# Kernel optimization log

Measured on AMD Instinct MI355X. Metric: run time of the kernel, lower is better.

Reference implementation:

```python
import jax, jax.numpy as jnp
import numpy as np

NUM_EXPERTS = 8
TOP_K = 2


def setup_inputs() -> dict:
    key = jax.random.key(0)
    ks = jax.random.split(key, 6)
    B, S, H, I, E = 2, 2048, 1024, 4096, NUM_EXPERTS
    scale_g = 1.0 / np.sqrt(H)
    scale1 = 1.0 / np.sqrt(H)
    scale2 = 1.0 / np.sqrt(I)
    return {
        "x": jax.random.normal(ks[0], (B, S, H), dtype=jnp.float32),
        "Wg": jax.random.normal(ks[1], (E, H), dtype=jnp.float32) * scale_g,
        "W1": jax.random.normal(ks[2], (E, I, H), dtype=jnp.float32) * scale1,
        "b1": jax.random.normal(ks[3], (E, I), dtype=jnp.float32) * scale1,
        "W2": jax.random.normal(ks[4], (E, H, I), dtype=jnp.float32) * scale2,
        "b2": jax.random.normal(ks[5], (E, H), dtype=jnp.float32) * scale2,
    }


def reference(x, Wg, W1, b1, W2, b2):
    # x: [B, S, H]
    B, S, H = x.shape
    flat = x.reshape(-1, H)  # [T, H], T = B*S

    # --- Router: gate logits -> softmax -> top-k -> renormalize ---
    logits = flat @ Wg.T                      # [T, E]
    probs = jax.nn.softmax(logits, axis=-1)   # [T, E]
    w, sel = jax.lax.top_k(probs, TOP_K)      # [T, K], [T, K]
    w = w / jnp.sum(w, axis=-1, keepdims=True)

    # --- Dispatch / expert MLP / weighted combine ---
    # Equivalent to argsort dispatch + per-expert chunks + combine:
    # each token receives sum_k w[t,k] * expert_{sel[t,k]}(flat[t]).
    out = jnp.zeros_like(flat)
    for e in range(NUM_EXPERTS):
        h = jax.nn.gelu(flat @ W1[e].T + b1[e], approximate=False)  # [T, I]
        y = h @ W2[e].T + b2[e]                                     # [T, H]
        we = jnp.sum(jnp.where(sel == e, w, 0.0), axis=-1)          # [T]
        out = out + we[:, None] * y
    return out.reshape(B, S, H)
```

## Files before the change

### kernel.cpp

```cpp
#include <hip/hip_runtime.h>
#include <hip/hip_bf16.h>
#include <math.h>

#define T_TOK 4096
#define H_DIM 1024
#define I_DIM 4096
#define NEXP 8
#define RMAX 8192

#if __has_builtin(__builtin_amdgcn_global_load_lds)
#define USE_GLL 1
#else
#define USE_GLL 0
#endif

typedef __attribute__((ext_vector_type(4))) float f32x4;
typedef __attribute__((ext_vector_type(8))) short short8;

#if USE_GLL
typedef __attribute__((address_space(1))) const void gconst_t;
typedef __attribute__((address_space(3))) void lds_t;
#endif

static __device__ __forceinline__ short bfc(float f) {
    return __builtin_bit_cast(short, __float2bfloat16(f));
}
static __device__ __forceinline__ short8 cvt8(float4 a, float4 b) {
    short8 r;
    r[0] = bfc(a.x); r[1] = bfc(a.y); r[2] = bfc(a.z); r[3] = bfc(a.w);
    r[4] = bfc(b.x); r[5] = bfc(b.y); r[6] = bfc(b.z); r[7] = bfc(b.w);
    return r;
}

#define W1_CHUNKS (NEXP * I_DIM * H_DIM / 8)
#define X_CHUNKS  (T_TOK * H_DIM / 8)

__global__ __launch_bounds__(256) void prep_kernel(
    const float* __restrict__ W1, const float* __restrict__ W2, const float* __restrict__ x,
    unsigned short* __restrict__ w1b, unsigned short* __restrict__ w2b, unsigned short* __restrict__ xb,
    int* __restrict__ counts)
{
    int stride = gridDim.x * blockDim.x;
    for (int i = blockIdx.x * blockDim.x + threadIdx.x; i < W1_CHUNKS; i += stride) {
        const float4* s1 = (const float4*)W1 + 2 * i;
        ((short8*)w1b)[i] = cvt8(s1[0], s1[1]);
        const float4* s2 = (const float4*)W2 + 2 * i;
        ((short8*)w2b)[i] = cvt8(s2[0], s2[1]);
        if (i < X_CHUNKS) {
            const float4* sx = (const float4*)x + 2 * i;
            ((short8*)xb)[i] = cvt8(sx[0], sx[1]);
        }
        if (i < 16) counts[i] = 0;
    }
}

__global__ __launch_bounds__(256) void router_kernel(
    const float* __restrict__ x, const float* __restrict__ Wg,
    int* __restrict__ sel, float* __restrict__ wtk, int* __restrict__ counts)
{
    __shared__ float wg[NEXP * H_DIM];
    int tid = threadIdx.x;
    float4* wg4 = (float4*)wg;
    const float4* Wg4 = (const float4*)Wg;
    for (int i = tid; i < NEXP * H_DIM / 4; i += 256) wg4[i] = Wg4[i];
    __syncthreads();

    int wid = tid >> 6, lane = tid & 63;
    int tok = blockIdx.x * 4 + wid;

    float acc[NEXP];
#pragma unroll
    for (int e = 0; e < NEXP; ++e) acc[e] = 0.f;

    const float* xr = x + tok * H_DIM;
#pragma unroll
    for (int it = 0; it < H_DIM / 64; ++it) {
        int h = it * 64 + lane;
        float xv = xr[h];
#pragma unroll
        for (int e = 0; e < NEXP; ++e) acc[e] += xv * wg[e * H_DIM + h];
    }
#pragma unroll
    for (int e = 0; e < NEXP; ++e) {
#pragma unroll
        for (int off = 32; off > 0; off >>= 1)
            acc[e] += __shfl_xor(acc[e], off);
    }
    if (lane == 0) {
        int e0 = 0; float l0 = acc[0];
#pragma unroll
        for (int e = 1; e < NEXP; ++e) if (acc[e] > l0) { l0 = acc[e]; e0 = e; }
        int e1 = -1; float l1 = -1e30f;
#pragma unroll
        for (int e = 0; e < NEXP; ++e) if (e != e0 && acc[e] > l1) { l1 = acc[e]; e1 = e; }
        float w0 = 1.f / (1.f + expf(l1 - l0));
        float w1 = 1.f - w0;
        sel[tok * 2 + 0] = e0; sel[tok * 2 + 1] = e1;
        wtk[tok * 2 + 0] = w0; wtk[tok * 2 + 1] = w1;
        atomicAdd(&counts[e0], 1);
        atomicAdd(&counts[e1], 1);
    }
}

__global__ void offsets_kernel(const int* __restrict__ counts, int* __restrict__ offsets) {
    if (threadIdx.x == 0) {
        int s = 0;
        for (int e = 0; e < NEXP; ++e) { offsets[e] = s; s += counts[e]; }
        offsets[NEXP] = s;
    }
}

__global__ void scatter_kernel(const int* __restrict__ sel,
                               const int* __restrict__ offsets, int* __restrict__ cursors,
                               int* __restrict__ rowTok, int* __restrict__ rowOfTok)
{
    int idx = blockIdx.x * blockDim.x + threadIdx.x;
    if (idx >= 2 * T_TOK) return;
    int t = idx >> 1;
    int e = sel[idx];
    int pos = atomicAdd(&cursors[e], 1);
    int row = offsets[e] + pos;
    rowTok[row] = t;
    rowOfTok[idx] = row;
}


__global__ __launch_bounds__(256) void gemm1_kernel(
    const unsigned short* __restrict__ xb, const unsigned short* __restrict__ w1b,
    const float* __restrict__ b1,
    const int* __restrict__ offsets, const int* __restrict__ rowTok,
    unsigned short* __restrict__ hbuf)
{
    int e = blockIdx.z;
    int rowBeg = offsets[e], rowEnd = offsets[e + 1];
    int mbase = rowBeg + blockIdx.y * 128;
    if (mbase >= rowEnd) return;
    int ntile = blockIdx.x;

    __shared__ __align__(16) short As[128 * 64];
    __shared__ __align__(16) short Bs[128 * 64];

    int tid = threadIdx.x;
    int wid = tid >> 6, lane = tid & 63;
    int wr = wid >> 1, wc = wid & 1;
    f32x4 acc[4][4] = {};

#if USE_GLL
    const unsigned short* aSrc[4];
    const unsigned short* bSrc[4];
#pragma unroll
    for (int i = 0; i < 4; ++i) {
        int cc = i * 64 + lane;
        int r = wid * 32 + (cc >> 3);
        int s = cc & 7;
        int chunk = s ^ (r & 7);
        int crow = min(mbase + r, rowEnd - 1);
        aSrc[i] = xb + (size_t)rowTok[crow] * H_DIM + chunk * 8;
        bSrc[i] = w1b + (size_t)e * (I_DIM * H_DIM) + (size_t)(ntile * 128 + r) * H_DIM + chunk * 8;
    }
    short* aDst = As + wid * 2048;
    short* bDst = Bs + wid * 2048;
#else
    int srow = tid >> 1, shalf = tid & 1;
    int crow = min(mbase + srow, rowEnd - 1);
    const unsigned short* aBase = xb + (size_t)rowTok[crow] * H_DIM + shalf * 32;
    const unsigned short* bBase = w1b + (size_t)e * (I_DIM * H_DIM) + (size_t)(ntile * 128 + srow) * H_DIM + shalf * 32;
#endif

    for (int kt = 0; kt < H_DIM / 64; ++kt) {
#if USE_GLL
#pragma unroll
        for (int i = 0; i < 4; ++i) {
            __builtin_amdgcn_global_load_lds((gconst_t*)(aSrc[i] + kt * 64), (lds_t*)(aDst + i * 512), 16, 0, 0);
            __builtin_amdgcn_global_load_lds((gconst_t*)(bSrc[i] + kt * 64), (lds_t*)(bDst + i * 512), 16, 0, 0);
        }
        __syncthreads();
#else
        short8 avv[4], bvv[4];
#pragma unroll
        for (int c = 0; c < 4; ++c) {
            avv[c] = ((const short8*)(aBase + kt * 64))[c];
            bvv[c] = ((const short8*)(bBase + kt * 64))[c];
        }
        __syncthreads();
#pragma unroll
        for (int c = 0; c < 4; ++c) {
            int sw = ((shalf * 4 + c) ^ (srow & 7)) << 4;
            *(short8*)((char*)As + srow * 128 + sw) = avv[c];
            *(short8*)((char*)Bs + srow * 128 + sw) = bvv[c];
        }
        __syncthreads();
#endif
#pragma unroll
        for (int ks = 0; ks < 2; ++ks) {
            short8 af[4], bfr[4];
            int kchunk = ks * 4 + (lane >> 4);
#pragma unroll
            for (int m = 0; m < 4; ++m) {
                int r = wr * 64 + m * 16 + (lane & 15);
                af[m] = *(const short8*)((const char*)As + r * 128 + ((kchunk ^ (r & 7)) << 4));
            }
#pragma unroll
            for (int n = 0; n < 4; ++n) {
                int r = wc * 64 + n * 16 + (lane & 15);
                bfr[n] = *(const short8*)((const char*)Bs + r * 128 + ((kchunk ^ (r & 7)) << 4));
            }
#pragma unroll
            for (int m = 0; m < 4; ++m)
#pragma unroll
                for (int n = 0; n < 4; ++n)
                    acc[m][n] = __builtin_amdgcn_mfma_f32_16x16x32_bf16(af[m], bfr[n], acc[m][n], 0, 0, 0);
        }
        __syncthreads();
    }

    const float* b1e = b1 + e * I_DIM + ntile * 128;
#pragma unroll
    for (int n = 0; n < 4; ++n) {
        int colL = wc * 64 + n * 16 + (lane & 15);
        float bias = b1e[colL];
        int colG = ntile * 128 + colL;
#pragma unroll
        for (int m = 0; m < 4; ++m) {
            int baseR = mbase + wr * 64 + m * 16 + ((lane >> 4) << 2);
            f32x4 f = acc[m][n];
#pragma unroll
            for (int j = 0; j < 4; ++j) {
                int r = baseR + j;
                if (r < rowEnd) {
                    float v = f[j] + bias;
                    v = 0.5f * v * (1.f + erff(v * 0.70710678118654752f));
                    hbuf[(size_t)r * I_DIM + colG] = (unsigned short)bfc(v);
                }
            }
        }
    }
}

__global__ __launch_bounds__(256) void gemm2_kernel(
    const unsigned short* __restrict__ hbuf, const unsigned short* __restrict__ w2b,
    const float* __restrict__ b2,
    const int* __restrict__ offsets,
    float* __restrict__ ybuf)
{
    int e = blockIdx.z;
    int rowBeg = offsets[e], rowEnd = offsets[e + 1];
    int mbase = rowBeg + blockIdx.y * 128;
    if (mbase >= rowEnd) return;
    int ntile = blockIdx.x;

    __shared__ __align__(16) short As[128 * 64];
    __shared__ __align__(16) short Bs[128 * 64];

    int tid = threadIdx.x;
    int wid = tid >> 6, lane = tid & 63;
    int wr = wid >> 1, wc = wid & 1;
    f32x4 acc[4][4] = {};

#if USE_GLL
    const unsigned short* aSrc[4];
    const unsigned short* bSrc[4];
#pragma unroll
    for (int i = 0; i < 4; ++i) {
        int cc = i * 64 + lane;
        int r = wid * 32 + (cc >> 3);
        int s = cc & 7;
        int chunk = s ^ (r & 7);
        int crow = min(mbase + r, rowEnd - 1);
        aSrc[i] = hbuf + (size_t)crow * I_DIM + chunk * 8;
        bSrc[i] = w2b + (size_t)e * (H_DIM * I_DIM) + (size_t)(ntile * 128 + r) * I_DIM + chunk * 8;
    }
    short* aDst = As + wid * 2048;
    short* bDst = Bs + wid * 2048;
#else
    int srow = tid >> 1, shalf = tid & 1;
    int crow = min(mbase + srow, rowEnd - 1);
    const unsigned short* aBase = hbuf + (size_t)crow * I_DIM + shalf * 32;
    const unsigned short* bBase = w2b + (size_t)e * (H_DIM * I_DIM) + (size_t)(ntile * 128 + srow) * I_DIM + shalf * 32;
#endif

    for (int kt = 0; kt < I_DIM / 64; ++kt) {
#if USE_GLL
#pragma unroll
        for (int i = 0; i < 4; ++i) {
            __builtin_amdgcn_global_load_lds((gconst_t*)(aSrc[i] + kt * 64), (lds_t*)(aDst + i * 512), 16, 0, 0);
            __builtin_amdgcn_global_load_lds((gconst_t*)(bSrc[i] + kt * 64), (lds_t*)(bDst + i * 512), 16, 0, 0);
        }
        __syncthreads();
#else
        short8 avv[4], bvv[4];
#pragma unroll
        for (int c = 0; c < 4; ++c) {
            avv[c] = ((const short8*)(aBase + kt * 64))[c];
            bvv[c] = ((const short8*)(bBase + kt * 64))[c];
        }
        __syncthreads();
#pragma unroll
        for (int c = 0; c < 4; ++c) {
            int sw = ((shalf * 4 + c) ^ (srow & 7)) << 4;
            *(short8*)((char*)As + srow * 128 + sw) = avv[c];
            *(short8*)((char*)Bs + srow * 128 + sw) = bvv[c];
        }
        __syncthreads();
#endif
#pragma unroll
        for (int ks = 0; ks < 2; ++ks) {
            short8 af[4], bfr[4];
            int kchunk = ks * 4 + (lane >> 4);
#pragma unroll
            for (int m = 0; m < 4; ++m) {
                int r = wr * 64 + m * 16 + (lane & 15);
                af[m] = *(const short8*)((const char*)As + r * 128 + ((kchunk ^ (r & 7)) << 4));
            }
#pragma unroll
            for (int n = 0; n < 4; ++n) {
                int r = wc * 64 + n * 16 + (lane & 15);
                bfr[n] = *(const short8*)((const char*)Bs + r * 128 + ((kchunk ^ (r & 7)) << 4));
            }
#pragma unroll
            for (int m = 0; m < 4; ++m)
#pragma unroll
                for (int n = 0; n < 4; ++n)
                    acc[m][n] = __builtin_amdgcn_mfma_f32_16x16x32_bf16(af[m], bfr[n], acc[m][n], 0, 0, 0);
        }
        __syncthreads();
    }

    const float* b2e = b2 + e * H_DIM + ntile * 128;
#pragma unroll
    for (int m = 0; m < 4; ++m) {
        int baseR = mbase + wr * 64 + m * 16 + ((lane >> 4) << 2);
#pragma unroll
        for (int n = 0; n < 4; ++n) {
            int colL = wc * 64 + n * 16 + (lane & 15);
            float bias = b2e[colL];
            int colG = ntile * 128 + colL;
            f32x4 f = acc[m][n];
#pragma unroll
            for (int j = 0; j < 4; ++j) {
                int r = baseR + j;
                if (r < rowEnd)
                    ybuf[(size_t)r * H_DIM + colG] = f[j] + bias;
            }
        }
    }
}

__global__ __launch_bounds__(256) void combine_kernel(
    const float* __restrict__ ybuf, const int* __restrict__ rowOfTok,
    const float* __restrict__ wtk, float* __restrict__ out)
{
    int t = blockIdx.x;
    int r0 = rowOfTok[2 * t], r1 = rowOfTok[2 * t + 1];
    float w0 = wtk[2 * t], w1 = wtk[2 * t + 1];
    const float4* y0 = (const float4*)(ybuf + (size_t)r0 * H_DIM);
    const float4* y1 = (const float4*)(ybuf + (size_t)r1 * H_DIM);
    float4* o = (float4*)(out + (size_t)t * H_DIM);
    int c = threadIdx.x;
    float4 a = y0[c], b = y1[c];
    float4 r;
    r.x = w0 * a.x + w1 * b.x;
    r.y = w0 * a.y + w1 * b.y;
    r.z = w0 * a.z + w1 * b.z;
    r.w = w0 * a.w + w1 * b.w;
    o[c] = r;
}

extern "C" void kernel_launch(void* const* d_in, const int* in_sizes, int n_in,
                              void* d_out, int out_size, void* d_ws, size_t ws_size,
                              hipStream_t stream) {
    const float* x  = (const float*)d_in[0];
    const float* Wg = (const float*)d_in[1];
    const float* W1 = (const float*)d_in[2];
    const float* b1 = (const float*)d_in[3];
    const float* W2 = (const float*)d_in[4];
    const float* b2 = (const float*)d_in[5];
    float* out = (float*)d_out;

    int* sel       = (int*)d_ws;
    float* wtk     = (float*)(sel + 2 * T_TOK);
    int* counts    = (int*)(wtk + 2 * T_TOK);
    int* cursors   = counts + 8;
    int* offsets   = cursors + 8;
    int* rowTok    = offsets + 16;
    int* rowOfTok  = rowTok + RMAX;
    unsigned short* xb   = (unsigned short*)(rowOfTok + RMAX);
    unsigned short* w1b  = xb + (size_t)T_TOK * H_DIM;
    unsigned short* w2b  = w1b + (size_t)NEXP * I_DIM * H_DIM;
    unsigned short* hbuf = w2b + (size_t)NEXP * H_DIM * I_DIM;
    float* ybuf          = (float*)(hbuf + (size_t)RMAX * I_DIM);

    prep_kernel<<<2048, 256, 0, stream>>>(W1, W2, x, w1b, w2b, xb, counts);
    router_kernel<<<T_TOK / 4, 256, 0, stream>>>(x, Wg, sel, wtk, counts);
    offsets_kernel<<<1, 64, 0, stream>>>(counts, offsets);
    scatter_kernel<<<(2 * T_TOK + 255) / 256, 256, 0, stream>>>(sel, offsets, cursors, rowTok, rowOfTok);
    gemm1_kernel<<<dim3(I_DIM / 128, 64, NEXP), 256, 0, stream>>>(xb, w1b, b1, offsets, rowTok, hbuf);
    gemm2_kernel<<<dim3(H_DIM / 128, 64, NEXP), 256, 0, stream>>>(hbuf, w2b, b2, offsets, ybuf);
    combine_kernel<<<T_TOK, 256, 0, stream>>>(ybuf, rowOfTok, wtk, out);
}
```

Before: 847.9 us.

## Double-buffer LDS tiles in expert GEMMs to overlap loads with MFMA

Both expert GEMM kernels now use two LDS buffers per operand. The next K-tile is prefetched, via global_load_lds or through registers, while MFMAs run on the current tile, which hides global load latency and removes one barrier per iteration on the GLL path. LDS use per block doubles to 64KB, which can lower occupancy. The prep kernel grid is also doubled.

Measured after the change: 849.3 us. Within noise of the previous version (+0.2%).

```diff
diff --git a/kernel.cpp b/kernel.cpp
--- a/kernel.cpp
+++ b/kernel.cpp
@@ -137,8 +137,8 @@
     if (mbase >= rowEnd) return;
     int ntile = blockIdx.x;
 
-    __shared__ __align__(16) short As[128 * 64];
-    __shared__ __align__(16) short Bs[128 * 64];
+    __shared__ __align__(16) short As[2][128 * 64];
+    __shared__ __align__(16) short Bs[2][128 * 64];
 
     int tid = threadIdx.x;
     int wid = tid >> 6, lane = tid & 63;
@@ -158,39 +158,55 @@
         aSrc[i] = xb + (size_t)rowTok[crow] * H_DIM + chunk * 8;
         bSrc[i] = w1b + (size_t)e * (I_DIM * H_DIM) + (size_t)(ntile * 128 + r) * H_DIM + chunk * 8;
     }
-    short* aDst = As + wid * 2048;
-    short* bDst = Bs + wid * 2048;
+#pragma unroll
+    for (int i = 0; i < 4; ++i) {
+        __builtin_amdgcn_global_load_lds((gconst_t*)aSrc[i], (lds_t*)(As[0] + wid * 2048 + i * 512), 16, 0, 0);
+        __builtin_amdgcn_global_load_lds((gconst_t*)bSrc[i], (lds_t*)(Bs[0] + wid * 2048 + i * 512), 16, 0, 0);
+    }
+    __syncthreads();
 #else
     int srow = tid >> 1, shalf = tid & 1;
-    int crow = min(mbase + srow, rowEnd - 1);
-    const unsigned short* aBase = xb + (size_t)rowTok[crow] * H_DIM + shalf * 32;
+    int crow0 = min(mbase + srow, rowEnd - 1);
+    const unsigned short* aBase = xb + (size_t)rowTok[crow0] * H_DIM + shalf * 32;
     const unsigned short* bBase = w1b + (size_t)e * (I_DIM * H_DIM) + (size_t)(ntile * 128 + srow) * H_DIM + shalf * 32;
-#endif
-
-    for (int kt = 0; kt < H_DIM / 64; ++kt) {
+    {
+        short8 avv[4], bvv[4];
+#pragma unroll
+        for (int c = 0; c < 4; ++c) { avv[c] = ((const short8*)aBase)[c]; bvv[c] = ((const short8*)bBase)[c]; }
+#pragma unroll
+        for (int c = 0; c < 4; ++c) {
+            int sw = ((shalf * 4 + c) ^ (srow & 7)) << 4;
+            *(short8*)((char*)As[0] + srow * 128 + sw) = avv[c];
+            *(short8*)((char*)Bs[0] + srow * 128 + sw) = bvv[c];
+        }
+        __syncthreads();
+    }
+#endif
+
+    const int NT = H_DIM / 64;
+    for (int kt = 0; kt < NT; ++kt) {
+        int cur = kt & 1;
 #if USE_GLL
-#pragma unroll
-        for (int i = 0; i < 4; ++i) {
-            __builtin_amdgcn_global_load_lds((gconst_t*)(aSrc[i] + kt * 64), (lds_t*)(aDst + i * 512), 16, 0, 0);
-            __builtin_amdgcn_global_load_lds((gconst_t*)(bSrc[i] + kt * 64), (lds_t*)(bDst + i * 512), 16, 0, 0);
-        }
-        __syncthreads();
+        if (kt + 1 < NT) {
+            int nxt = cur ^ 1;
+#pragma unroll
+            for (int i = 0; i < 4; ++i) {
+                __builtin_amdgcn_global_load_lds((gconst_t*)(aSrc[i] + (kt + 1) * 64), (lds_t*)(As[nxt] + wid * 2048 + i * 512), 16, 0, 0);
+                __builtin_amdgcn_global_load_lds((gconst_t*)(bSrc[i] + (kt + 1) * 64), (lds_t*)(Bs[nxt] + wid * 2048 + i * 512), 16, 0, 0);
+            }
+        }
 #else
         short8 avv[4], bvv[4];
-#pragma unroll
-        for (int c = 0; c < 4; ++c) {
-            avv[c] = ((const short8*)(aBase + kt * 64))[c];
-            bvv[c] = ((const short8*)(bBase + kt * 64))[c];
-        }
-        __syncthreads();
-#pragma unroll
-        for (int c = 0; c < 4; ++c) {
-            int sw = ((shalf * 4 + c) ^ (srow & 7)) << 4;
-            *(short8*)((char*)As + srow * 128 + sw) = avv[c];
-            *(short8*)((char*)Bs + srow * 128 + sw) = bvv[c];
-        }
-        __syncthreads();
-#endif
+        if (kt + 1 < NT) {
+#pragma unroll
+            for (int c = 0; c < 4; ++c) {
+                avv[c] = ((const short8*)(aBase + (kt + 1) * 64))[c];
+                bvv[c] = ((const short8*)(bBase + (kt + 1) * 64))[c];
+            }
+        }
+#endif
+        const short* curA = As[cur];
+        const short* curB = Bs[cur];
 #pragma unroll
         for (int ks = 0; ks < 2; ++ks) {
             short8 af[4], bfr[4];
@@ -198,12 +214,12 @@
 #pragma unroll
             for (int m = 0; m < 4; ++m) {
                 int r = wr * 64 + m * 16 + (lane & 15);
-                af[m] = *(const short8*)((const char*)As + r * 128 + ((kchunk ^ (r & 7)) << 4));
+                af[m] = *(const short8*)((const char*)curA + r * 128 + ((kchunk ^ (r & 7)) << 4));
             }
 #pragma unroll
             for (int n = 0; n < 4; ++n) {
                 int r = wc * 64 + n * 16 + (lane & 15);
-                bfr[n] = *(const short8*)((const char*)Bs + r * 128 + ((kchunk ^ (r & 7)) << 4));
+                bfr[n] = *(const short8*)((const char*)curB + r * 128 + ((kchunk ^ (r & 7)) << 4));
             }
 #pragma unroll
             for (int m = 0; m < 4; ++m)
@@ -211,6 +227,18 @@
                 for (int n = 0; n < 4; ++n)
                     acc[m][n] = __builtin_amdgcn_mfma_f32_16x16x32_bf16(af[m], bfr[n], acc[m][n], 0, 0, 0);
         }
+#if !USE_GLL
+        if (kt + 1 < NT) {
+            __syncthreads();
+            int nxt = cur ^ 1;
+#pragma unroll
+            for (int c = 0; c < 4; ++c) {
+                int sw = ((shalf * 4 + c) ^ (srow & 7)) << 4;
+                *(short8*)((char*)As[nxt] + srow * 128 + sw) = avv[c];
+                *(short8*)((char*)Bs[nxt] + srow * 128 + sw) = bvv[c];
+            }
+        }
+#endif
         __syncthreads();
     }
 
@@ -249,8 +277,8 @@
     if (mbase >= rowEnd) return;
     int ntile = blockIdx.x;
 
-    __shared__ __align__(16) short As[128 * 64];
-    __shared__ __align__(16) short Bs[128 * 64];
+    __shared__ __align__(16) short As[2][128 * 64];
+    __shared__ __align__(16) short Bs[2][128 * 64];
 
     int tid = threadIdx.x;
     int wid = tid >> 6, lane = tid & 63;
@@ -270,39 +298,55 @@
         aSrc[i] = hbuf + (size_t)crow * I_DIM + chunk * 8;
         bSrc[i] = w2b + (size_t)e * (H_DIM * I_DIM) + (size_t)(ntile * 128 + r) * I_DIM + chunk * 8;
     }
-    short* aDst = As + wid * 2048;
-    short* bDst = Bs + wid * 2048;
+#pragma unroll
+    for (int i = 0; i < 4; ++i) {
+        __builtin_amdgcn_global_load_lds((gconst_t*)aSrc[i], (lds_t*)(As[0] + wid * 2048 + i * 512), 16, 0, 0);
+        __builtin_amdgcn_global_load_lds((gconst_t*)bSrc[i], (lds_t*)(Bs[0] + wid * 2048 + i * 512), 16, 0, 0);
+    }
+    __syncthreads();
 #else
     int srow = tid >> 1, shalf = tid & 1;
-    int crow = min(mbase + srow, rowEnd - 1);
-    const unsigned short* aBase = hbuf + (size_t)crow * I_DIM + shalf * 32;
+    int crow0 = min(mbase + srow, rowEnd - 1);
+    const unsigned short* aBase = hbuf + (size_t)crow0 * I_DIM + shalf * 32;
     const unsigned short* bBase = w2b + (size_t)e * (H_DIM * I_DIM) + (size_t)(ntile * 128 + srow) * I_DIM + shalf * 32;
-#endif
-
-    for (int kt = 0; kt < I_DIM / 64; ++kt) {
+    {
+        short8 avv[4], bvv[4];
+#pragma unroll
+        for (int c = 0; c < 4; ++c) { avv[c] = ((const short8*)aBase)[c]; bvv[c] = ((const short8*)bBase)[c]; }
+#pragma unroll
+        for (int c = 0; c < 4; ++c) {
+            int sw = ((shalf * 4 + c) ^ (srow & 7)) << 4;
+            *(short8*)((char*)As[0] + srow * 128 + sw) = avv[c];
+            *(short8*)((char*)Bs[0] + srow * 128 + sw) = bvv[c];
+        }
+        __syncthreads();
+    }
+#endif
+
+    const int NT = I_DIM / 64;
+    for (int kt = 0; kt < NT; ++kt) {
+        int cur = kt & 1;
 #if USE_GLL
-#pragma unroll
-        for (int i = 0; i < 4; ++i) {
-            __builtin_amdgcn_global_load_lds((gconst_t*)(aSrc[i] + kt * 64), (lds_t*)(aDst + i * 512), 16, 0, 0);
-            __builtin_amdgcn_global_load_lds((gconst_t*)(bSrc[i] + kt * 64), (lds_t*)(bDst + i * 512), 16, 0, 0);
-        }
-        __syncthreads();
+        if (kt + 1 < NT) {
+            int nxt = cur ^ 1;
+#pragma unroll
+            for (int i = 0; i < 4; ++i) {
+                __builtin_amdgcn_global_load_lds((gconst_t*)(aSrc[i] + (kt + 1) * 64), (lds_t*)(As[nxt] + wid * 2048 + i * 512), 16, 0, 0);
+                __builtin_amdgcn_global_load_lds((gconst_t*)(bSrc[i] + (kt + 1) * 64), (lds_t*)(Bs[nxt] + wid * 2048 + i * 512), 16, 0, 0);
+            }
+        }
 #else
         short8 avv[4], bvv[4];
-#pragma unroll
-        for (int c = 0; c < 4; ++c) {
-            avv[c] = ((const short8*)(aBase + kt * 64))[c];
-            bvv[c] = ((const short8*)(bBase + kt * 64))[c];
-        }
-        __syncthreads();
-#pragma unroll
-        for (int c = 0; c < 4; ++c) {
-            int sw = ((shalf * 4 + c) ^ (srow & 7)) << 4;
-            *(short8*)((char*)As + srow * 128 + sw) = avv[c];
-            *(short8*)((char*)Bs + srow * 128 + sw) = bvv[c];
-        }
-        __syncthreads();
-#endif
+        if (kt + 1 < NT) {
+#pragma unroll
+            for (int c = 0; c < 4; ++c) {
+                avv[c] = ((const short8*)(aBase + (kt + 1) * 64))[c];
+                bvv[c] = ((const short8*)(bBase + (kt + 1) * 64))[c];
+            }
+        }
+#endif
+        const short* curA = As[cur];
+        const short* curB = Bs[cur];
 #pragma unroll
         for (int ks = 0; ks < 2; ++ks) {
             short8 af[4], bfr[4];
@@ -310,12 +354,12 @@
 #pragma unroll
             for (int m = 0; m < 4; ++m) {
                 int r = wr * 64 + m * 16 + (lane & 15);
-                af[m] = *(const short8*)((const char*)As + r * 128 + ((kchunk ^ (r & 7)) << 4));
+                af[m] = *(const short8*)((const char*)curA + r * 128 + ((kchunk ^ (r & 7)) << 4));
             }
 #pragma unroll
             for (int n = 0; n < 4; ++n) {
                 int r = wc * 64 + n * 16 + (lane & 15);
-                bfr[n] = *(const short8*)((const char*)Bs + r * 128 + ((kchunk ^ (r & 7)) << 4));
+                bfr[n] = *(const short8*)((const char*)curB + r * 128 + ((kchunk ^ (r & 7)) << 4));
             }
 #pragma unroll
             for (int m = 0; m < 4; ++m)
@@ -323,6 +367,18 @@
                 for (int n = 0; n < 4; ++n)
                     acc[m][n] = __builtin_amdgcn_mfma_f32_16x16x32_bf16(af[m], bfr[n], acc[m][n], 0, 0, 0);
         }
+#if !USE_GLL
+        if (kt + 1 < NT) {
+            __syncthreads();
+            int nxt = cur ^ 1;
+#pragma unroll
+            for (int c = 0; c < 4; ++c) {
+                int sw = ((shalf * 4 + c) ^ (srow & 7)) << 4;
+                *(short8*)((char*)As[nxt] + srow * 128 + sw) = avv[c];
+                *(short8*)((char*)Bs[nxt] + srow * 128 + sw) = bvv[c];
+            }
+        }
+#endif
         __syncthreads();
     }
 
@@ -390,7 +446,7 @@
     unsigned short* hbuf = w2b + (size_t)NEXP * H_DIM * I_DIM;
     float* ybuf          = (float*)(hbuf + (size_t)RMAX * I_DIM);
 
-    prep_kernel<<<2048, 256, 0, stream>>>(W1, W2, x, w1b, w2b, xb, counts);
+    prep_kernel<<<4096, 256, 0, stream>>>(W1, W2, x, w1b, w2b, xb, counts);
     router_kernel<<<T_TOK / 4, 256, 0, stream>>>(x, Wg, sel, wtk, counts);
     offsets_kernel<<<1, 64, 0, stream>>>(counts, offsets);
     scatter_kernel<<<(2 * T_TOK + 255) / 256, 256, 0, stream>>>(sel, offsets, cursors, rowTok, rowOfTok);
```
